# Kernel optimization log

Hardware: AMD Instinct MI355X
Metric: run time of the kernel (lower is better)

The kernel has to match this reference:

```python
import jax, jax.numpy as jnp
import numpy as np

N = 100_000      # nodes
E = 3_200_000    # edges
B = 1024         # graphs in batch
IN = 4           # in_channels
G = 16           # GCNNodes
D = 32           # NDenseNodes


def _linear_params(k, out_f, in_f):
    s = 1.0 / np.sqrt(in_f)
    kw, kb = jax.random.split(k)
    W = jax.random.uniform(kw, (out_f, in_f), jnp.float32, -s, s)
    b = jax.random.uniform(kb, (out_f,), jnp.float32, -s, s)
    return W, b


def setup_inputs() -> dict:
    key = jax.random.key(0)
    ks = jax.random.split(key, 12)
    X = jax.random.normal(ks[0], (N, IN), jnp.float32)
    Edge_index = jax.random.randint(ks[1], (2, E), 0, N, jnp.int64)
    Edge_weight = jax.random.uniform(ks[2], (E,), jnp.float32)
    Batching = jnp.sort(jax.random.randint(ks[3], (N,), 0, B, jnp.int64))
    W1, b1 = _linear_params(ks[4], G, IN)   # Conv1 lin (PyG GCNConv: Linear no bias + bias param)
    W2, b2 = _linear_params(ks[5], G, G)    # Conv2
    C1w, C1b = _linear_params(ks[6], D, 2 * G)
    C2w, C2b = _linear_params(ks[7], D, D)
    C3w, C3b = _linear_params(ks[8], 1, D)
    R1w, R1b = _linear_params(ks[9], D, 2 * G)
    R2w, R2b = _linear_params(ks[10], D, D)
    R3w, R3b = _linear_params(ks[11], 1, D)
    return {"X": X, "Edge_index": Edge_index, "Edge_weight": Edge_weight,
            "Batching": Batching, "num_graphs": B,
            "W1": W1, "b1": b1, "W2": W2, "b2": b2,
            "C1w": C1w, "C1b": C1b, "C2w": C2w, "C2b": C2b, "C3w": C3w, "C3b": C3b,
            "R1w": R1w, "R1b": R1b, "R2w": R2w, "R2b": R2b, "R3w": R3w, "R3b": R3b}


def _gcn_conv(x, row, col, w, W, b):
    """PyG GCNConv: add self loops (weight 1), symmetric norm, x@W.T, scatter-add at col, +b."""
    n = x.shape[0]
    loop = jnp.arange(n)
    row2 = jnp.concatenate([row, loop])
    col2 = jnp.concatenate([col, loop])
    w2 = jnp.concatenate([w, jnp.ones((n,), x.dtype)])
    deg = jax.ops.segment_sum(w2, col2, num_segments=n)          # deg >= 1 via self loops
    dinv = jnp.where(deg > 0, jax.lax.rsqrt(deg), 0.0)
    norm = dinv[row2] * w2 * dinv[col2]                           # [E+n]
    xw = x @ W.T                                                  # [n, out]
    out = jax.ops.segment_sum(norm[:, None] * xw[row2], col2, num_segments=n)
    return out + b


def reference(X, Edge_index, Edge_weight, Batching, num_graphs,
              W1, b1, W2, b2, C1w, C1b, C2w, C2b, C3w, C3b,
              R1w, R1b, R2w, R2b, R3w, R3b):
    act = jax.nn.leaky_relu  # default slope 0.01, matches nn.LeakyReLU()
    row, col = Edge_index[0], Edge_index[1]
    # add_self_loops then keep only col > row  ==  zero out weights where col <= row
    w = jnp.where(col > row, Edge_weight, 0.0)

    out = act(_gcn_conv(X, row, col, w, W1, b1))
    out = act(_gcn_conv(out, row, col, w, W2, b2))

    ones = jnp.ones((out.shape[0],), out.dtype)
    cnt = jax.ops.segment_sum(ones, Batching, num_segments=num_graphs)
    outMean = jax.ops.segment_sum(out, Batching, num_segments=num_graphs) / jnp.maximum(cnt, 1.0)[:, None]
    outMax = jax.ops.segment_max(out, Batching, num_segments=num_graphs)
    pooled = jnp.concatenate([outMean, outMax], axis=1)           # [B, 2G]

    Chi0 = act(pooled @ C1w.T + C1b)
    Chi0 = act(Chi0 @ C2w.T + C2b)
    Chi0 = Chi0 @ C3w.T + C3b
    Rp = act(pooled @ R1w.T + R1b)
    Rp = act(Rp @ R2w.T + R2b)
    Rp = Rp @ R3w.T + R3b
    return jnp.concatenate([Chi0, Rp], axis=1)                    # [B, 2]
```

## Files before the change

### kernel.cpp

```cpp
#include <hip/hip_runtime.h>
#include <hip/hip_bf16.h>
#include <float.h>

#define LRELU(x) ((x) > 0.0f ? (x) : 0.01f * (x))

typedef unsigned long long u64;
#define MASK40 (((u64)1 << 40) - 1)

__global__ __launch_bounds__(256) void k_zero(u64* __restrict__ deg64, int N) {
    int i = blockIdx.x * blockDim.x + threadIdx.x;
    if (i < N) deg64[i] = (u64)1 << 32;
}

__global__ __launch_bounds__(256) void k_countx(const int* __restrict__ row,
                                                const int* __restrict__ col,
                                                const float* __restrict__ w,
                                                const float* __restrict__ X,
                                                const float* __restrict__ W1,
                                                u64* __restrict__ deg64,
                                                unsigned char* __restrict__ rank,
                                                float* __restrict__ xw1,
                                                int E, int N, int gE) {
    int tid = threadIdx.x;
    if ((int)blockIdx.x < gE) {
        int e = blockIdx.x * 256 + tid;
        if (e >= E) return;
        int r = row[e], c = col[e];
        if (c <= r) return;
        u64 add = ((u64)1 << 40) | (u64)(w[e] * 4294967296.0f);
        u64 old = atomicAdd(deg64 + c, add);
        rank[e] = (unsigned char)(old >> 40);
    } else {
        int i = (blockIdx.x - gE) * 256 + tid;
        if (i >= N) return;
        const float4 x = *reinterpret_cast<const float4*>(X + 4 * i);
        float o[16];
#pragma unroll
        for (int g = 0; g < 16; ++g) {
            const float4 wr = *reinterpret_cast<const float4*>(W1 + 4 * g);
            o[g] = x.x * wr.x + x.y * wr.y + x.z * wr.z + x.w * wr.w;
        }
        float4* dst = reinterpret_cast<float4*>(xw1 + 16 * i);
#pragma unroll
        for (int k = 0; k < 4; ++k)
            dst[k] = make_float4(o[4 * k], o[4 * k + 1], o[4 * k + 2], o[4 * k + 3]);
    }
}

__global__ __launch_bounds__(256) void k_scan1(const u64* __restrict__ deg64,
                                               int* __restrict__ offs,
                                               int* __restrict__ partials,
                                               float* __restrict__ dinv, int N) {
    __shared__ int sm[256];
    int tid = threadIdx.x;
    int base = blockIdx.x * 1024 + tid * 4;
    int v[4];
    float dv[4];
    int s = 0;
#pragma unroll
    for (int k = 0; k < 4; ++k) {
        int idx = base + k;
        u64 d = (idx < N) ? deg64[idx] : ((u64)1 << 32);
        v[k] = (int)(d >> 40);
        float wsum = (float)((double)(d & MASK40) * (1.0 / 4294967296.0));
        dv[k] = rsqrtf(wsum);
        s += v[k];
    }
    if (base + 3 < N) {
        *reinterpret_cast<float4*>(dinv + base) = make_float4(dv[0], dv[1], dv[2], dv[3]);
    } else {
#pragma unroll
        for (int k = 0; k < 4; ++k) if (base + k < N) dinv[base + k] = dv[k];
    }
    sm[tid] = s;
    __syncthreads();
    for (int off = 1; off < 256; off <<= 1) {
        int t = (tid >= off) ? sm[tid - off] : 0;
        __syncthreads();
        sm[tid] += t;
        __syncthreads();
    }
    int run = sm[tid] - s;
#pragma unroll
    for (int k = 0; k < 4; ++k) {
        int idx = base + k;
        if (idx < N) offs[idx] = run;
        run += v[k];
    }
    if (tid == 255) partials[blockIdx.x] = sm[255];
}

__global__ __launch_bounds__(256) void k_scan2(int* __restrict__ partials,
                                               int* __restrict__ offs, int nb, int N) {
    __shared__ int sm[256];
    int tid = threadIdx.x;
    int v = (tid < nb) ? partials[tid] : 0;
    sm[tid] = v;
    __syncthreads();
    for (int off = 1; off < 256; off <<= 1) {
        int t = (tid >= off) ? sm[tid - off] : 0;
        __syncthreads();
        sm[tid] += t;
        __syncthreads();
    }
    if (tid < nb) partials[tid] = sm[tid] - v;
    if (tid == nb - 1) offs[N] = sm[tid];
}

__global__ __launch_bounds__(256) void k_fillx(const int* __restrict__ row,
                                               const int* __restrict__ col,
                                               const float* __restrict__ w,
                                               const float* __restrict__ dinv,
                                               const int* __restrict__ offs,
                                               const int* __restrict__ part,
                                               const unsigned char* __restrict__ rank,
                                               int2* __restrict__ pack,
                                               int* __restrict__ offsF,
                                               int E, int N, int gE) {
    int tid = threadIdx.x;
    if ((int)blockIdx.x < gE) {
        int e = blockIdx.x * 256 + tid;
        if (e >= E) return;
        int r = row[e], c = col[e];
        if (c <= r) return;
        float nrm = dinv[r] * w[e] * dinv[c];
        int pos = offs[c] + part[c >> 10] + (int)rank[e];
        pack[pos] = make_int2(r, __float_as_int(nrm));
    } else {
        int i = (blockIdx.x - gE) * 256 + tid;
        if (i == 0) offsF[N] = offs[N];
        if (i >= N) return;
        offsF[i] = offs[i] + part[i >> 10];
    }
}

__global__ __launch_bounds__(256) void k_gather1m(const int* __restrict__ offsF,
                                                  const int2* __restrict__ pack,
                                                  const float* __restrict__ xw1,
                                                  const float* __restrict__ dinv,
                                                  const float* __restrict__ b1,
                                                  const float* __restrict__ W2,
                                                  float* __restrict__ xw2, int N) {
    int t = blockIdx.x * blockDim.x + threadIdx.x;
    int NT = 16 * N;
    bool valid = t < NT;
    int tc = valid ? t : NT - 1;
    int c = tc >> 4, g = tc & 15;
    int beg = offsF[c], end = offsF[c + 1];
    float d = dinv[c];
    float a = d * d * xw1[tc];
    for (int j = beg; j < end; ++j) {
        int2 p = pack[j];
        a += __int_as_float(p.y) * xw1[((size_t)p.x << 4) + g];
    }
    float h = a + b1[g];
    h = LRELU(h);
    int lane = threadIdx.x & 63;
    int base = lane & 48;
    const float4* W2r = reinterpret_cast<const float4*>(W2 + 16 * g);
    float4 w0 = W2r[0], w1 = W2r[1], w2 = W2r[2], w3 = W2r[3];
    float o = 0.0f;
    o += __shfl(h, base + 0) * w0.x;
    o += __shfl(h, base + 1) * w0.y;
    o += __shfl(h, base + 2) * w0.z;
    o += __shfl(h, base + 3) * w0.w;
    o += __shfl(h, base + 4) * w1.x;
    o += __shfl(h, base + 5) * w1.y;
    o += __shfl(h, base + 6) * w1.z;
    o += __shfl(h, base + 7) * w1.w;
    o += __shfl(h, base + 8) * w2.x;
    o += __shfl(h, base + 9) * w2.y;
    o += __shfl(h, base + 10) * w2.z;
    o += __shfl(h, base + 11) * w2.w;
    o += __shfl(h, base + 12) * w3.x;
    o += __shfl(h, base + 13) * w3.y;
    o += __shfl(h, base + 14) * w3.z;
    o += __shfl(h, base + 15) * w3.w;
    if (valid) xw2[t] = o;
}

__global__ __launch_bounds__(256) void k_gather2(const int* __restrict__ offsF,
                                                 const int2* __restrict__ pack,
                                                 const float* __restrict__ xw2,
                                                 const float* __restrict__ dinv,
                                                 const float* __restrict__ b2,
                                                 float* __restrict__ acc, int N) {
    int t = blockIdx.x * blockDim.x + threadIdx.x;
    if (t >= 16 * N) return;
    int c = t >> 4, g = t & 15;
    int beg = offsF[c], end = offsF[c + 1];
    float d = dinv[c];
    float a = d * d * xw2[t];
    for (int j = beg; j < end; ++j) {
        int2 p = pack[j];
        a += __int_as_float(p.y) * xw2[((size_t)p.x << 4) + g];
    }
    a += b2[g];
    acc[t] = LRELU(a);
}

__global__ __launch_bounds__(64) void k_poolA(const float* __restrict__ acc,
                                              const int* __restrict__ batching,
                                              int N,
                                              const float* __restrict__ C1w, const float* __restrict__ C1b,
                                              const float* __restrict__ C2w, const float* __restrict__ C2b,
                                              const float* __restrict__ C3w, const float* __restrict__ C3b,
                                              const float* __restrict__ R1w, const float* __restrict__ R1b,
                                              const float* __restrict__ R2w, const float* __restrict__ R2b,
                                              const float* __restrict__ R3w, const float* __restrict__ R3b,
                                              float* __restrict__ out) {
    int b = blockIdx.x;
    int t = threadIdx.x;
    __shared__ int s_se[2];
    __shared__ float sp[32];
    __shared__ float h1s[64];
    __shared__ float h2s[64];
    if (t < 2) {
        int target = b + t;
        int lo = 0, hi = N;
        while (lo < hi) {
            int mid = (lo + hi) >> 1;
            if (batching[mid] < target) lo = mid + 1; else hi = mid;
        }
        s_se[t] = lo;
    }
    __syncthreads();
    int start = s_se[0], end = s_se[1];
    int g = t & 15, sub = t >> 4;
    float sum = 0.0f, mx = -FLT_MAX;
    for (int n = start + sub; n < end; n += 4) {
        float v = acc[16 * n + g];
        sum += v;
        mx = fmaxf(mx, v);
    }
    sum += __shfl_down(sum, 32);
    mx = fmaxf(mx, __shfl_down(mx, 32));
    sum += __shfl_down(sum, 16);
    mx = fmaxf(mx, __shfl_down(mx, 16));
    if (t < 16) {
        float cnt = (float)(end - start);
        sp[t] = sum / fmaxf(cnt, 1.0f);
        sp[16 + t] = mx;
    }
    __syncthreads();
    int d = t & 31;
    const float* W1h = (t < 32) ? C1w : R1w;
    const float* b1h = (t < 32) ? C1b : R1b;
    float a1 = b1h[d];
#pragma unroll 4
    for (int k = 0; k < 32; ++k) a1 += sp[k] * W1h[32 * d + k];
    h1s[t] = LRELU(a1);
    __syncthreads();
    const float* W2h = (t < 32) ? C2w : R2w;
    const float* b2h = (t < 32) ? C2b : R2b;
    const float* h1base = h1s + (t < 32 ? 0 : 32);
    float a2 = b2h[d];
#pragma unroll 4
    for (int k = 0; k < 32; ++k) a2 += h1base[k] * W2h[32 * d + k];
    h2s[t] = LRELU(a2);
    __syncthreads();
    if (t == 0 || t == 32) {
        const float* w3 = (t == 0) ? C3w : R3w;
        float a3 = (t == 0) ? C3b[0] : R3b[0];
        const float* hb = h2s + t;
#pragma unroll 4
        for (int k = 0; k < 32; ++k) a3 += hb[k] * w3[k];
        out[2 * b + (t >> 5)] = a3;
    }
}

__global__ __launch_bounds__(256) void k_initf(const float* __restrict__ X,
                                               const float* __restrict__ W1,
                                               float* __restrict__ deg,
                                               float* __restrict__ xw, int N) {
    int i = blockIdx.x * blockDim.x + threadIdx.x;
    if (i >= N) return;
    deg[i] = 1.0f;
    const float4 x = *reinterpret_cast<const float4*>(X + 4 * i);
    float o[16];
#pragma unroll
    for (int g = 0; g < 16; ++g) {
        const float4 wr = *reinterpret_cast<const float4*>(W1 + 4 * g);
        o[g] = x.x * wr.x + x.y * wr.y + x.z * wr.z + x.w * wr.w;
    }
    float4* dst = reinterpret_cast<float4*>(xw + 16 * i);
#pragma unroll
    for (int k = 0; k < 4; ++k)
        dst[k] = make_float4(o[4 * k], o[4 * k + 1], o[4 * k + 2], o[4 * k + 3]);
}

__global__ __launch_bounds__(256) void k_degf(const int* __restrict__ row,
                                              const int* __restrict__ col,
                                              const float* __restrict__ w,
                                              float* __restrict__ deg, int E) {
    int e = blockIdx.x * blockDim.x + threadIdx.x;
    if (e >= E) return;
    int r = row[e], c = col[e];
    if (c > r) atomicAdd(deg + c, w[e]);
}

__global__ __launch_bounds__(256) void k_self(float* __restrict__ deg_dinv,
                                              const float* __restrict__ xw,
                                              float* __restrict__ acc, int N) {
    int i = blockIdx.x * blockDim.x + threadIdx.x;
    if (i >= N) return;
    float d = rsqrtf(deg_dinv[i]);
    deg_dinv[i] = d;
    float s = d * d;
    const float4* xs = reinterpret_cast<const float4*>(xw + 16 * i);
    float4* as = reinterpret_cast<float4*>(acc + 16 * i);
#pragma unroll
    for (int k = 0; k < 4; ++k) {
        float4 v = xs[k];
        as[k] = make_float4(s * v.x, s * v.y, s * v.z, s * v.w);
    }
}

__global__ __launch_bounds__(256) void k_scatter(const int* __restrict__ row,
                                                 const int* __restrict__ col,
                                                 const float* __restrict__ w,
                                                 const float* __restrict__ dinv,
                                                 const float* __restrict__ xw,
                                                 float* __restrict__ acc, int E) {
    int e = blockIdx.x * blockDim.x + threadIdx.x;
    if (e >= E) return;
    int r = row[e], c = col[e];
    if (c <= r) return;
    float nrm = dinv[r] * w[e] * dinv[c];
    const float4* xr = reinterpret_cast<const float4*>(xw + 16 * r);
    float* ac = acc + 16 * c;
#pragma unroll
    for (int k = 0; k < 4; ++k) {
        float4 v = xr[k];
        atomicAdd(ac + 4 * k + 0, nrm * v.x);
        atomicAdd(ac + 4 * k + 1, nrm * v.y);
        atomicAdd(ac + 4 * k + 2, nrm * v.z);
        atomicAdd(ac + 4 * k + 3, nrm * v.w);
    }
}

__global__ __launch_bounds__(256) void k_mid(const float* __restrict__ b1,
                                             const float* __restrict__ W2,
                                             const float* __restrict__ dinv,
                                             float* __restrict__ xw,
                                             float* __restrict__ acc, int N) {
    int i = blockIdx.x * blockDim.x + threadIdx.x;
    if (i >= N) return;
    float h[16];
#pragma unroll
    for (int g = 0; g < 16; ++g) {
        float v = acc[16 * i + g] + b1[g];
        h[g] = LRELU(v);
    }
    float d = dinv[i];
    float s = d * d;
#pragma unroll
    for (int g = 0; g < 16; ++g) {
        float a = 0.0f;
#pragma unroll
        for (int k = 0; k < 16; ++k) a += h[k] * W2[16 * g + k];
        xw[16 * i + g] = a;
        acc[16 * i + g] = s * a;
    }
}

__global__ __launch_bounds__(256) void k_act(const float* __restrict__ b2,
                                             float* __restrict__ acc, int NT) {
    int t = blockIdx.x * blockDim.x + threadIdx.x;
    if (t >= NT) return;
    float v = acc[t] + b2[t & 15];
    acc[t] = LRELU(v);
}

extern "C" void kernel_launch(void* const* d_in, const int* in_sizes, int n_in,
                              void* d_out, int out_size, void* d_ws, size_t ws_size,
                              hipStream_t stream) {
    const float* X   = (const float*)d_in[0];
    const int*   EI  = (const int*)d_in[1];
    const float* EW  = (const float*)d_in[2];
    const int*   Bat = (const int*)d_in[3];
    const float* W1  = (const float*)d_in[5];
    const float* b1  = (const float*)d_in[6];
    const float* W2  = (const float*)d_in[7];
    const float* b2  = (const float*)d_in[8];
    const float* C1w = (const float*)d_in[9];
    const float* C1b = (const float*)d_in[10];
    const float* C2w = (const float*)d_in[11];
    const float* C2b = (const float*)d_in[12];
    const float* C3w = (const float*)d_in[13];
    const float* C3b = (const float*)d_in[14];
    const float* R1w = (const float*)d_in[15];
    const float* R1b = (const float*)d_in[16];
    const float* R2w = (const float*)d_in[17];
    const float* R2b = (const float*)d_in[18];
    const float* R3w = (const float*)d_in[19];
    const float* R3b = (const float*)d_in[20];

    const int N = in_sizes[0] / 4;
    const int E = in_sizes[1] / 2;
    const int B = out_size / 2;
    const int* row = EI;
    const int* col = EI + E;

    float* outp = (float*)d_out;

    size_t off = 0;
    u64*   deg64 = (u64*)d_ws;            off += 2 * (size_t)N;
    float* xw1   = (float*)d_ws + off;    off += 16 * (size_t)N;
    float* xw2   = (float*)d_ws + off;    off += 16 * (size_t)N;
    float* dinv  = (float*)d_ws + off;    off += (size_t)N;
    int*   offs  = (int*)d_ws + off;      off += (size_t)N + 1;
    int*   offsF = (int*)d_ws + off;      off += (size_t)N + 1;
    int*   part  = (int*)d_ws + off;      off += 256;
    unsigned char* rank = (unsigned char*)((int*)d_ws + off);
    off += ((size_t)E + 3) / 4;
    off = (off + 1) & ~(size_t)1;
    int2*  pack  = (int2*)((int*)d_ws + off);
    size_t needed = off * 4 + (size_t)E * 8;

    const int nb = (N + 1023) / 1024;

    dim3 blk(256);
    const int gN  = (N + 255) / 256;
    const int gE  = (E + 255) / 256;
    const int gNG = (16 * N + 255) / 256;

    if (needed <= ws_size && nb <= 256) {
        float* acc = xw1;
        k_zero  <<<dim3(gN), blk, 0, stream>>>(deg64, N);
        k_countx<<<dim3(gE + gN), blk, 0, stream>>>(row, col, EW, X, W1,
                                                    deg64, rank, xw1, E, N, gE);
        k_scan1 <<<dim3(nb), blk, 0, stream>>>(deg64, offs, part, dinv, N);
        k_scan2 <<<dim3(1), blk, 0, stream>>>(part, offs, nb, N);
        k_fillx <<<dim3(gE + gN), blk, 0, stream>>>(row, col, EW, dinv, offs, part,
                                                    rank, pack, offsF, E, N, gE);
        k_gather1m<<<dim3(gNG), blk, 0, stream>>>(offsF, pack, xw1, dinv, b1, W2, xw2, N);
        k_gather2 <<<dim3(gNG), blk, 0, stream>>>(offsF, pack, xw2, dinv, b2, acc, N);
        k_poolA <<<dim3(B), dim3(64), 0, stream>>>(acc, Bat, N,
                                                   C1w, C1b, C2w, C2b, C3w, C3b,
                                                   R1w, R1b, R2w, R2b, R3w, R3b,
                                                   outp);
    } else {
        float* deg = (float*)d_ws;
        float* xw  = (float*)d_ws + N;
        float* acc = xw + 16 * (size_t)N;
        k_initf<<<dim3(gN), blk, 0, stream>>>(X, W1, deg, xw, N);
        k_degf <<<dim3(gE), blk, 0, stream>>>(row, col, EW, deg, E);
        k_self <<<dim3(gN), blk, 0, stream>>>(deg, xw, acc, N);
        k_scatter<<<dim3(gE), blk, 0, stream>>>(row, col, EW, deg, xw, acc, E);
        k_mid  <<<dim3(gN), blk, 0, stream>>>(b1, W2, deg, xw, acc, N);
        k_scatter<<<dim3(gE), blk, 0, stream>>>(row, col, EW, deg, xw, acc, E);
        k_act  <<<dim3(gNG), blk, 0, stream>>>(b2, acc, 16 * N);
        k_poolA<<<dim3(B), dim3(64), 0, stream>>>(acc, Bat, N,
                                                  C1w, C1b, C2w, C2b, C3w, C3b,
                                                  R1w, R1b, R2w, R2b, R3w, R3b,
                                                  outp);
    }
}
```

Measured before the change: 252.5 us.

## Compact active edges during counting and fold degree normalization into features

```diff
diff --git a/kernel.cpp b/kernel.cpp
--- a/kernel.cpp
+++ b/kernel.cpp
@@ -4,12 +4,18 @@
 
 #define LRELU(x) ((x) > 0.0f ? (x) : 0.01f * (x))
 
+typedef unsigned int u32;
 typedef unsigned long long u64;
-#define MASK40 (((u64)1 << 40) - 1)
-
-__global__ __launch_bounds__(256) void k_zero(u64* __restrict__ deg64, int N) {
+
+#define WSUM_ONE   (1u << 17)
+#define WSUM_MASK  ((1u << 25) - 1)
+#define CNT_ONE    (1u << 25)
+
+__global__ __launch_bounds__(256) void k_zero(u32* __restrict__ deg32,
+                                              int* __restrict__ cursor, int N) {
     int i = blockIdx.x * blockDim.x + threadIdx.x;
-    if (i < N) deg64[i] = (u64)1 << 32;
+    if (i < N) deg32[i] = WSUM_ONE;
+    if (i == 0) *cursor = 0;
 }
 
 __global__ __launch_bounds__(256) void k_countx(const int* __restrict__ row,
@@ -17,19 +23,44 @@
                                                 const float* __restrict__ w,
                                                 const float* __restrict__ X,
                                                 const float* __restrict__ W1,
-                                                u64* __restrict__ deg64,
-                                                unsigned char* __restrict__ rank,
+                                                u32* __restrict__ deg32,
+                                                int* __restrict__ cursor,
+                                                int2* __restrict__ cpk,
+                                                int* __restrict__ meta,
                                                 float* __restrict__ xw1,
-                                                int E, int N, int gE) {
+                                                int E, int N, int gE, int cap) {
     int tid = threadIdx.x;
     if ((int)blockIdx.x < gE) {
         int e = blockIdx.x * 256 + tid;
-        if (e >= E) return;
-        int r = row[e], c = col[e];
-        if (c <= r) return;
-        u64 add = ((u64)1 << 40) | (u64)(w[e] * 4294967296.0f);
-        u64 old = atomicAdd(deg64 + c, add);
-        rank[e] = (unsigned char)(old >> 40);
+        int r = 0, c = 0; float wv = 0.0f;
+        bool act = false;
+        if (e < E) {
+            r = row[e]; c = col[e];
+            if (c > r) { act = true; wv = w[e]; }
+        }
+        u64 m = __ballot(act);
+        int lane = tid & 63, wvi = tid >> 6;
+        int pre = __popcll(m & (((u64)1 << lane) - 1));
+        int tot = __popcll(m);
+        __shared__ int wsum_s[4];
+        __shared__ int base_s;
+        if (lane == 0) wsum_s[wvi] = tot;
+        __syncthreads();
+        if (tid == 0)
+            base_s = atomicAdd(cursor, wsum_s[0] + wsum_s[1] + wsum_s[2] + wsum_s[3]);
+        __syncthreads();
+        int woff = 0;
+#pragma unroll
+        for (int k = 0; k < 3; ++k) if (k < wvi) woff += wsum_s[k];
+        if (act) {
+            u32 add = CNT_ONE | (u32)(wv * 131072.0f);
+            u32 old = atomicAdd(deg32 + c, add);
+            int pos = base_s + woff + pre;
+            if (pos < cap) {
+                cpk[pos] = make_int2(r, __float_as_int(wv));
+                meta[pos] = (c << 7) | (int)(old >> 25);
+            }
+        }
     } else {
         int i = (blockIdx.x - gE) * 256 + tid;
         if (i >= N) return;
@@ -47,10 +78,11 @@
     }
 }
 
-__global__ __launch_bounds__(256) void k_scan1(const u64* __restrict__ deg64,
+__global__ __launch_bounds__(256) void k_scan1(const u32* __restrict__ deg32,
                                                int* __restrict__ offs,
                                                int* __restrict__ partials,
-                                               float* __restrict__ dinv, int N) {
+                                               float* __restrict__ dinv,
+                                               float* __restrict__ xw, int N) {
     __shared__ int sm[256];
     int tid = threadIdx.x;
     int base = blockIdx.x * 1024 + tid * 4;
@@ -60,17 +92,37 @@
 #pragma unroll
     for (int k = 0; k < 4; ++k) {
         int idx = base + k;
-        u64 d = (idx < N) ? deg64[idx] : ((u64)1 << 32);
-        v[k] = (int)(d >> 40);
-        float wsum = (float)((double)(d & MASK40) * (1.0 / 4294967296.0));
-        dv[k] = rsqrtf(wsum);
+        u32 d = (idx < N) ? deg32[idx] : WSUM_ONE;
+        v[k] = (int)(d >> 25);
+        dv[k] = rsqrtf((float)(d & WSUM_MASK) * (1.0f / 131072.0f));
         s += v[k];
     }
     if (base + 3 < N) {
         *reinterpret_cast<float4*>(dinv + base) = make_float4(dv[0], dv[1], dv[2], dv[3]);
+#pragma unroll
+        for (int k = 0; k < 4; ++k) {
+            float4* p = reinterpret_cast<float4*>(xw + 16 * (base + k));
+            float sc = dv[k];
+#pragma unroll
+            for (int q = 0; q < 4; ++q) {
+                float4 t = p[q];
+                p[q] = make_float4(sc * t.x, sc * t.y, sc * t.z, sc * t.w);
+            }
+        }
     } else {
 #pragma unroll
-        for (int k = 0; k < 4; ++k) if (base + k < N) dinv[base + k] = dv[k];
+        for (int k = 0; k < 4; ++k) {
+            if (base + k < N) {
+                dinv[base + k] = dv[k];
+                float4* p = reinterpret_cast<float4*>(xw + 16 * (base + k));
+                float sc = dv[k];
+#pragma unroll
+                for (int q = 0; q < 4; ++q) {
+                    float4 t = p[q];
+                    p[q] = make_float4(sc * t.x, sc * t.y, sc * t.z, sc * t.w);
+                }
+            }
+        }
     }
     sm[tid] = s;
     __syncthreads();
@@ -107,27 +159,24 @@
     if (tid == nb - 1) offs[N] = sm[tid];
 }
 
-__global__ __launch_bounds__(256) void k_fillx(const int* __restrict__ row,
-                                               const int* __restrict__ col,
-                                               const float* __restrict__ w,
-                                               const float* __restrict__ dinv,
+__global__ __launch_bounds__(256) void k_fillx(const int2* __restrict__ cpk,
+                                               const int* __restrict__ meta,
+                                               const int* __restrict__ cursor,
                                                const int* __restrict__ offs,
                                                const int* __restrict__ part,
-                                               const unsigned char* __restrict__ rank,
                                                int2* __restrict__ pack,
                                                int* __restrict__ offsF,
-                                               int E, int N, int gE) {
+                                               int N, int gP) {
     int tid = threadIdx.x;
-    if ((int)blockIdx.x < gE) {
-        int e = blockIdx.x * 256 + tid;
-        if (e >= E) return;
-        int r = row[e], c = col[e];
-        if (c <= r) return;
-        float nrm = dinv[r] * w[e] * dinv[c];
-        int pos = offs[c] + part[c >> 10] + (int)rank[e];
-        pack[pos] = make_int2(r, __float_as_int(nrm));
+    if ((int)blockIdx.x < gP) {
+        int i = blockIdx.x * 256 + tid;
+        if (i >= *cursor) return;
+        int m = meta[i];
+        int c = m >> 7;
+        int pos = offs[c] + part[c >> 10] + (m & 127);
+        pack[pos] = cpk[i];
     } else {
-        int i = (blockIdx.x - gE) * 256 + tid;
+        int i = (blockIdx.x - gP) * 256 + tid;
         if (i == 0) offsF[N] = offs[N];
         if (i >= N) return;
         offsF[i] = offs[i] + part[i >> 10];
@@ -136,11 +185,11 @@
 
 __global__ __launch_bounds__(256) void k_gather1m(const int* __restrict__ offsF,
                                                   const int2* __restrict__ pack,
-                                                  const float* __restrict__ xw1,
+                                                  const float* __restrict__ xs1,
                                                   const float* __restrict__ dinv,
                                                   const float* __restrict__ b1,
                                                   const float* __restrict__ W2,
-                                                  float* __restrict__ xw2, int N) {
+                                                  float* __restrict__ xs2, int N) {
     int t = blockIdx.x * blockDim.x + threadIdx.x;
     int NT = 16 * N;
     bool valid = t < NT;
@@ -148,12 +197,12 @@
     int c = tc >> 4, g = tc & 15;
     int beg = offsF[c], end = offsF[c + 1];
     float d = dinv[c];
-    float a = d * d * xw1[tc];
+    float s = xs1[tc];
     for (int j = beg; j < end; ++j) {
         int2 p = pack[j];
-        a += __int_as_float(p.y) * xw1[((size_t)p.x << 4) + g];
-    }
-    float h = a + b1[g];
+        s += __int_as_float(p.y) * xs1[((size_t)p.x << 4) + g];
+    }
+    float h = d * s + b1[g];
     h = LRELU(h);
     int lane = threadIdx.x & 63;
     int base = lane & 48;
@@ -176,12 +225,12 @@
     o += __shfl(h, base + 13) * w3.y;
     o += __shfl(h, base + 14) * w3.z;
     o += __shfl(h, base + 15) * w3.w;
-    if (valid) xw2[t] = o;
+    if (valid) xs2[t] = d * o;
 }
 
 __global__ __launch_bounds__(256) void k_gather2(const int* __restrict__ offsF,
                                                  const int2* __restrict__ pack,
-                                                 const float* __restrict__ xw2,
+                                                 const float* __restrict__ xs2,
                                                  const float* __restrict__ dinv,
                                                  const float* __restrict__ b2,
                                                  float* __restrict__ acc, int N) {
@@ -190,12 +239,12 @@
     int c = t >> 4, g = t & 15;
     int beg = offsF[c], end = offsF[c + 1];
     float d = dinv[c];
-    float a = d * d * xw2[t];
+    float s = xs2[t];
     for (int j = beg; j < end; ++j) {
         int2 p = pack[j];
-        a += __int_as_float(p.y) * xw2[((size_t)p.x << 4) + g];
-    }
-    a += b2[g];
+        s += __int_as_float(p.y) * xs2[((size_t)p.x << 4) + g];
+    }
+    float a = d * s + b2[g];
     acc[t] = LRELU(a);
 }
 
@@ -404,38 +453,43 @@
 
     float* outp = (float*)d_out;
 
+    const int CAP = E / 2 + 16384;
+
     size_t off = 0;
-    u64*   deg64 = (u64*)d_ws;            off += 2 * (size_t)N;
-    float* xw1   = (float*)d_ws + off;    off += 16 * (size_t)N;
-    float* xw2   = (float*)d_ws + off;    off += 16 * (size_t)N;
+    u32*   deg32 = (u32*)d_ws;            off += (size_t)N;
+    float* xs1   = (float*)d_ws + off;    off += 16 * (size_t)N;
+    float* xs2   = (float*)d_ws + off;    off += 16 * (size_t)N;
     float* dinv  = (float*)d_ws + off;    off += (size_t)N;
     int*   offs  = (int*)d_ws + off;      off += (size_t)N + 1;
     int*   offsF = (int*)d_ws + off;      off += (size_t)N + 1;
     int*   part  = (int*)d_ws + off;      off += 256;
-    unsigned char* rank = (unsigned char*)((int*)d_ws + off);
-    off += ((size_t)E + 3) / 4;
+    int*   cursor= (int*)d_ws + off;      off += 2;
+    int*   meta  = (int*)d_ws + off;      off += (size_t)CAP;
     off = (off + 1) & ~(size_t)1;
-    int2*  pack  = (int2*)((int*)d_ws + off);
-    size_t needed = off * 4 + (size_t)E * 8;
+    int2*  cpk   = (int2*)((int*)d_ws + off); off += 2 * (size_t)CAP;
+    int2*  pack  = (int2*)((int*)d_ws + off); off += 2 * (size_t)CAP;
+    size_t needed = off * 4;
 
     const int nb = (N + 1023) / 1024;
 
     dim3 blk(256);
     const int gN  = (N + 255) / 256;
     const int gE  = (E + 255) / 256;
+    const int gP  = (CAP + 255) / 256;
     const int gNG = (16 * N + 255) / 256;
 
     if (needed <= ws_size && nb <= 256) {
-        float* acc = xw1;
-        k_zero  <<<dim3(gN), blk, 0, stream>>>(deg64, N);
+        float* acc = xs1;
+        k_zero  <<<dim3(gN), blk, 0, stream>>>(deg32, cursor, N);
         k_countx<<<dim3(gE + gN), blk, 0, stream>>>(row, col, EW, X, W1,
-                                                    deg64, rank, xw1, E, N, gE);
-        k_scan1 <<<dim3(nb), blk, 0, stream>>>(deg64, offs, part, dinv, N);
+                                                    deg32, cursor, cpk, meta, xs1,
+                                                    E, N, gE, CAP);
+        k_scan1 <<<dim3(nb), blk, 0, stream>>>(deg32, offs, part, dinv, xs1, N);
         k_scan2 <<<dim3(1), blk, 0, stream>>>(part, offs, nb, N);
-        k_fillx <<<dim3(gE + gN), blk, 0, stream>>>(row, col, EW, dinv, offs, part,
-                                                    rank, pack, offsF, E, N, gE);
-        k_gather1m<<<dim3(gNG), blk, 0, stream>>>(offsF, pack, xw1, dinv, b1, W2, xw2, N);
-        k_gather2 <<<dim3(gNG), blk, 0, stream>>>(offsF, pack, xw2, dinv, b2, acc, N);
+        k_fillx <<<dim3(gP + gN), blk, 0, stream>>>(cpk, meta, cursor, offs, part,
+                                                    pack, offsF, N, gP);
+        k_gather1m<<<dim3(gNG), blk, 0, stream>>>(offsF, pack, xs1, dinv, b1, W2, xs2, N);
+        k_gather2 <<<dim3(gNG), blk, 0, stream>>>(offsF, pack, xs2, dinv, b2, acc, N);
         k_poolA <<<dim3(B), dim3(64), 0, stream>>>(acc, Bat, N,
                                                    C1w, C1b, C2w, C2b, C3w, C3b,
                                                    R1w, R1b, R2w, R2b, R3w, R3b,
```

Result: slower. 336.4 us (+33.3%).
